# Performance work log

Hardware: AMD Instinct MI355X
Metric: run time of the kernel (lower is better)

The kernel has to match this reference:

```python
import jax, jax.numpy as jnp
import numpy as np

BATCH_SIZE = 4096          # B; representation has 2B rows
TEMPERATURE = 0.5


def setup_inputs() -> dict:
    key = jax.random.key(0)
    k1, k2, k3 = jax.random.split(key, 3)
    representation = jax.random.normal(k1, (2 * BATCH_SIZE, 128), dtype=jnp.float32)
    xrecon = jax.random.normal(k2, (2 * BATCH_SIZE, 512), dtype=jnp.float32)
    xorig = jax.random.normal(k3, (2 * BATCH_SIZE, 512), dtype=jnp.float32)
    return {"representation": representation, "xrecon": xrecon, "xorig": xorig}


def _xneg_loss(representation, batch_size, temperature):
    # Cosine similarity matrix [2B, 2B]
    n = representation / (jnp.linalg.norm(representation, axis=-1, keepdims=True) + 1e-8)
    sim = n @ n.T  # [2B, 2B]
    sim = sim / temperature
    two_b = 2 * batch_size
    # Positives: diag(sim, +B) then diag(sim, -B) -> [2B]
    l_pos = jnp.diagonal(sim, offset=batch_size)
    r_pos = jnp.diagonal(sim, offset=-batch_size)
    positives = jnp.concatenate([l_pos, r_pos])  # [2B]
    # NT-Xent: logits row i = [pos_i] + (row i minus diag and minus pos entry).
    # The union of {pos_i} and negatives_i is row i with only the main diagonal
    # removed, so CE with label 0 equals: -pos_i + logsumexp(row_i \ {diag}).
    neg_inf = jnp.finfo(sim.dtype).min
    eye = jnp.eye(two_b, dtype=bool)
    sim_no_diag = jnp.where(eye, neg_inf, sim)
    lse = jax.nn.logsumexp(sim_no_diag, axis=1)  # [2B]
    loss_sum = jnp.sum(lse - positives)           # CrossEntropyLoss(reduction='sum')
    return loss_sum / two_b


def reference(representation, xrecon, xorig):
    # reconstruction=True -> MSELoss (mean reduction)
    recon_loss = jnp.mean((xrecon - xorig) ** 2)
    loss = recon_loss
    # contrastive_loss=True
    closs = _xneg_loss(representation, BATCH_SIZE, TEMPERATURE)
    loss = loss + closs
    # distance_loss=True: MSE between the two halves of representation
    zi, zj = representation[:BATCH_SIZE], representation[BATCH_SIZE:]
    zrecon_loss = jnp.mean((zi - zj) ** 2)
    loss = loss + zrecon_loss
    return (loss, closs, recon_loss, zrecon_loss)
```

## Files before the change

kernel.cpp:

```cpp
#include <hip/hip_runtime.h>
#include <math.h>

#define BATCH 4096
#define NROWS (2 * BATCH)
#define D 128
#define DX 512

constexpr int NSPLIT = 8;
constexpr int NT = 8;
constexpr int SLOTS = NSPLIT * 2;

#define SCALE 1.698644f

#define WS_PART   0
#define WS_RECONP 131072
#define WS_ZRECP  (WS_RECONP + 512)
#define WS_POSP   (WS_ZRECP + 256)
#define WS_LSEP   (WS_POSP + 256)
#define WS_NBF8   (WS_LSEP + 64)

typedef float f32x16 __attribute__((ext_vector_type(16)));
typedef long long i64;
typedef unsigned char u8;
typedef unsigned short u16;

__device__ __forceinline__ float wave_reduce(float v) {
    #pragma unroll
    for (int o = 32; o > 0; o >>= 1) v += __shfl_xor(v, o);
    return v;
}

__global__ __launch_bounds__(256) void k_prep(const float* __restrict__ rep,
                                              float* __restrict__ ws) {
    const int w = threadIdx.x >> 6, l = threadIdx.x & 63;
    const int wg = blockIdx.x * 4 + w;
    u8* nbf8 = (u8*)(ws + WS_NBF8);
    const int chunk = l >> 2, el = (l & 3) * 2;
    float zacc = 0.f, pacc = 0.f;
    #pragma unroll
    for (int p = 0; p < 4; ++p) {
        const int i = wg + p * 1024;
        float2 a = *reinterpret_cast<const float2*>(rep + i * D + l * 2);
        float2 b = *reinterpret_cast<const float2*>(rep + (i + BATCH) * D + l * 2);
        float dx = a.x - b.x, dy = a.y - b.y;
        float sa  = wave_reduce(a.x * a.x + a.y * a.y);
        float sb  = wave_reduce(b.x * b.x + b.y * b.y);
        float sab = wave_reduce(a.x * b.x + a.y * b.y);
        float sd  = wave_reduce(dx * dx + dy * dy);
        float ia = 1.0f / (sqrtf(sa) + 1e-8f);
        float ib = 1.0f / (sqrtf(sb) + 1e-8f);
        zacc += sd;
        pacc += sab * ia * ib;
        int pka = __builtin_amdgcn_cvt_pk_fp8_f32(a.x * ia * SCALE,
                                                  a.y * ia * SCALE, 0, false);
        int pkb = __builtin_amdgcn_cvt_pk_fp8_f32(b.x * ib * SCALE,
                                                  b.y * ib * SCALE, 0, false);
        *reinterpret_cast<u16*>(
            nbf8 + ((size_t)chunk * NROWS + i) * 8 + el) = (u16)pka;
        *reinterpret_cast<u16*>(
            nbf8 + ((size_t)chunk * NROWS + i + BATCH) * 8 + el) = (u16)pkb;
    }
    __shared__ float shz[4], shp[4];
    if (l == 0) { shz[w] = zacc; shp[w] = pacc; }
    __syncthreads();
    if (threadIdx.x == 0) {
        ws[WS_ZRECP + blockIdx.x] = shz[0] + shz[1] + shz[2] + shz[3];
        ws[WS_POSP + blockIdx.x] = 4.0f * (shp[0] + shp[1] + shp[2] + shp[3]);
    }
}

__global__ __launch_bounds__(256, 2) void k_lse(const float4* __restrict__ xr,
                                                const float4* __restrict__ xo,
                                                float* __restrict__ ws) {
    const u8* __restrict__ nbf8 = (const u8*)(ws + WS_NBF8);
    const int tid = threadIdx.x;
    const int w = tid >> 6, l = tid & 63;
    const int wr = w >> 1, wc = w & 1;
    const int rblk = blockIdx.x;
    const int split = blockIdx.y;
    const int R0 = rblk * 128;
    const int fid = rblk + 64 * split;

    i64 afrag[2][8];
    #pragma unroll
    for (int rb = 0; rb < 2; ++rb) {
        const int lr = R0 + wr * 64 + rb * 32 + (l & 31);
        #pragma unroll
        for (int s = 0; s < 8; ++s) {
            const int c = 2 * s + (l >> 5);
            afrag[rb][s] = *reinterpret_cast<const i64*>(
                nbf8 + ((size_t)c * NROWS + lr) * 8);
        }
    }

    i64 bufA[16], bufB[16];
    float4 raA, rbA, raB, rbB;
    float sumexp[2][16] = {};
    float racc = 0.f;

    auto loadB = [&](i64 (&buf)[16], int t) {
        const int lc = split * (NT * 128) + t * 128 + wc * 64 + (l & 31);
        #pragma unroll
        for (int s = 0; s < 8; ++s) {
            const int c = 2 * s + (l >> 5);
            const u8* base = nbf8 + (size_t)c * NROWS * 8;
            buf[2 * s]     = *reinterpret_cast<const i64*>(base + (size_t)lc * 8);
            buf[2 * s + 1] = *reinterpret_cast<const i64*>(base + (size_t)(lc + 32) * 8);
        }
    };

    auto tile = [&](i64 (&buf)[16], int t, float4 ra, float4 rb2) {
        const int C0 = split * (NT * 128) + t * 128;
        const bool diagt = (C0 == R0);
        f32x16 acc[2][2] = {};
        #pragma unroll
        for (int s = 0; s < 8; ++s) {
            acc[0][0] = __builtin_amdgcn_mfma_f32_32x32x16_fp8_fp8(
                afrag[0][s], buf[2 * s], acc[0][0], 0, 0, 0);
            acc[0][1] = __builtin_amdgcn_mfma_f32_32x32x16_fp8_fp8(
                afrag[0][s], buf[2 * s + 1], acc[0][1], 0, 0, 0);
            acc[1][0] = __builtin_amdgcn_mfma_f32_32x32x16_fp8_fp8(
                afrag[1][s], buf[2 * s], acc[1][0], 0, 0, 0);
            acc[1][1] = __builtin_amdgcn_mfma_f32_32x32x16_fp8_fp8(
                afrag[1][s], buf[2 * s + 1], acc[1][1], 0, 0, 0);
        }
        {
            float dx = ra.x - rb2.x, dy = ra.y - rb2.y;
            float dz = ra.z - rb2.z, dw2 = ra.w - rb2.w;
            racc += dx * dx + dy * dy + dz * dz + dw2 * dw2;
        }
        #pragma unroll
        for (int rb = 0; rb < 2; ++rb) {
            #pragma unroll
            for (int cb = 0; cb < 2; ++cb) {
                const bool dmask = diagt && ((2 * wr + rb) == (2 * wc + cb));
                #pragma unroll
                for (int r = 0; r < 16; ++r) {
                    float e = __builtin_amdgcn_exp2f(acc[rb][cb][r]);
                    if (dmask) {
                        const int rrow = (r & 3) + 8 * (r >> 2) + 4 * (l >> 5);
                        if (rrow == (l & 31)) e = 0.0f;
                    }
                    sumexp[rb][r] += e;
                }
            }
        }
    };

    loadB(bufA, 0);
    {
        const int ri = fid * 2048 + tid;
        raA = xr[ri]; rbA = xo[ri];
    }

    #pragma unroll
    for (int tt = 0; tt < NT; tt += 2) {
        if (tt + 1 < NT) {
            loadB(bufB, tt + 1);
            const int ri = fid * 2048 + (tt + 1) * 256 + tid;
            raB = xr[ri]; rbB = xo[ri];
        }
        tile(bufA, tt, raA, rbA);
        if (tt + 2 < NT) {
            loadB(bufA, tt + 2);
            const int ri = fid * 2048 + (tt + 2) * 256 + tid;
            raA = xr[ri]; rbA = xo[ri];
        }
        if (tt + 1 < NT) tile(bufB, tt + 1, raB, rbB);
    }

    #pragma unroll
    for (int rb = 0; rb < 2; ++rb) {
        #pragma unroll
        for (int r = 0; r < 16; ++r) {
            float v = sumexp[rb][r];
            #pragma unroll
            for (int m = 1; m <= 16; m <<= 1) v += __shfl_xor(v, m);
            sumexp[rb][r] = v;
        }
    }
    if ((l & 31) == 0) {
        #pragma unroll
        for (int rb = 0; rb < 2; ++rb) {
            #pragma unroll
            for (int r = 0; r < 16; ++r) {
                const int row = R0 + wr * 64 + rb * 32
                              + (r & 3) + 8 * (r >> 2) + 4 * (l >> 5);
                ws[WS_PART + row * SLOTS + split * 2 + wc] = sumexp[rb][r];
            }
        }
    }

    racc = wave_reduce(racc);
    __shared__ float shr[4];
    if (l == 0) shr[w] = racc;
    __syncthreads();
    if (tid == 0) ws[WS_RECONP + fid] = shr[0] + shr[1] + shr[2] + shr[3];
}

__global__ __launch_bounds__(256) void k_rowlse(float* __restrict__ ws) {
    const int q = blockIdx.x, tid = threadIdx.x;
    const int j = tid & 127, h = tid >> 7;
    const int row = q * 128 + j;
    float s = 0.f;
    #pragma unroll
    for (int ss = 0; ss < SLOTS / 2; ++ss)
        s += ws[WS_PART + row * SLOTS + 2 * ss + h];
    __shared__ float red[128];
    if (h) red[j] = s;
    __syncthreads();
    float lg = 0.f;
    if (!h) lg = logf(s + red[j]);
    lg = wave_reduce(lg);
    __shared__ float sh[4];
    const int w = tid >> 6, l = tid & 63;
    if (l == 0) sh[w] = lg;
    __syncthreads();
    if (tid == 0) ws[WS_LSEP + q] = sh[0] + sh[1] + sh[2] + sh[3];
}

__global__ __launch_bounds__(256) void k_combine(const float* __restrict__ ws,
                                                 float* __restrict__ out) {
    const int tid = threadIdx.x;
    float lacc = (tid < 64) ? ws[WS_LSEP + tid] : 0.f;
    float racc = ws[WS_RECONP + tid] + ws[WS_RECONP + 256 + tid];
    float zacc = ws[WS_ZRECP + tid];
    float pacc = ws[WS_POSP + tid];

    lacc = wave_reduce(lacc);
    racc = wave_reduce(racc);
    zacc = wave_reduce(zacc);
    pacc = wave_reduce(pacc);

    __shared__ float sh[4][4];
    const int w = tid >> 6, l = tid & 63;
    if (l == 0) { sh[0][w] = lacc; sh[1][w] = racc; sh[2][w] = zacc; sh[3][w] = pacc; }
    __syncthreads();
    if (tid == 0) {
        float lse = sh[0][0] + sh[0][1] + sh[0][2] + sh[0][3];
        float rec = (sh[1][0] + sh[1][1] + sh[1][2] + sh[1][3]) / (float)(NROWS * DX);
        float zre = (sh[2][0] + sh[2][1] + sh[2][2] + sh[2][3]) / (float)(BATCH * D);
        float pos = sh[3][0] + sh[3][1] + sh[3][2] + sh[3][3];
        float closs = (lse - pos) / (float)NROWS;
        out[0] = rec + closs + zre;
        out[1] = closs;
        out[2] = rec;
        out[3] = zre;
    }
}

extern "C" void kernel_launch(void* const* d_in, const int* in_sizes, int n_in,
                              void* d_out, int out_size, void* d_ws, size_t ws_size,
                              hipStream_t stream) {
    const float* rep = (const float*)d_in[0];
    const float4* xr = (const float4*)d_in[1];
    const float4* xo = (const float4*)d_in[2];
    float* out = (float*)d_out;
    float* ws = (float*)d_ws;

    k_prep<<<256, 256, 0, stream>>>(rep, ws);
    dim3 grid(64, NSPLIT);
    k_lse<<<grid, 256, 0, stream>>>(xr, xo, ws);
    k_rowlse<<<64, 256, 0, stream>>>(ws);
    k_combine<<<1, 256, 0, stream>>>(ws, out);
}
```

Before: 33.44 us.

## Software-pipeline MFMA and exp epilogue at half-tile granularity

Splits each 128-column tile into two 64-column halves, each with its own B-fragment buffer and accumulator pair. It interleaves the MFMAs of one half with the exp/sum epilogue of the previous half, so matrix and transcendental units overlap instead of running back to back. The B prefetch buffers shrink from 16 to 8 i64 each, but two live accumulator sets add register pressure under launch_bounds(256,2).

```diff
diff --git a/kernel.cpp b/kernel.cpp
--- a/kernel.cpp
+++ b/kernel.cpp
@@ -86,87 +86,86 @@
     for (int rb = 0; rb < 2; ++rb) {
         const int lr = R0 + wr * 64 + rb * 32 + (l & 31);
         #pragma unroll
-        for (int s = 0; s < 8; ++s) {
-            const int c = 2 * s + (l >> 5);
-            afrag[rb][s] = *reinterpret_cast<const i64*>(
+        for (int k = 0; k < 8; ++k) {
+            const int c = 2 * k + (l >> 5);
+            afrag[rb][k] = *reinterpret_cast<const i64*>(
                 nbf8 + ((size_t)c * NROWS + lr) * 8);
         }
     }
 
-    i64 bufA[16], bufB[16];
-    float4 raA, rbA, raB, rbB;
+    i64 bufA[8], bufB[8];
+    f32x16 accA[2], accB[2];
+    float4 ra, rb2;
     float sumexp[2][16] = {};
     float racc = 0.f;
 
-    auto loadB = [&](i64 (&buf)[16], int t) {
-        const int lc = split * (NT * 128) + t * 128 + wc * 64 + (l & 31);
-        #pragma unroll
-        for (int s = 0; s < 8; ++s) {
-            const int c = 2 * s + (l >> 5);
-            const u8* base = nbf8 + (size_t)c * NROWS * 8;
-            buf[2 * s]     = *reinterpret_cast<const i64*>(base + (size_t)lc * 8);
-            buf[2 * s + 1] = *reinterpret_cast<const i64*>(base + (size_t)(lc + 32) * 8);
+    auto loadB = [&](i64 (&buf)[8], int s) {
+        const int lc = split * (NT * 128) + (s >> 1) * 128 + wc * 64
+                     + (s & 1) * 32 + (l & 31);
+        #pragma unroll
+        for (int k = 0; k < 8; ++k) {
+            const int c = 2 * k + (l >> 5);
+            buf[k] = *reinterpret_cast<const i64*>(
+                nbf8 + ((size_t)c * NROWS + lc) * 8);
         }
     };
 
-    auto tile = [&](i64 (&buf)[16], int t, float4 ra, float4 rb2) {
-        const int C0 = split * (NT * 128) + t * 128;
-        const bool diagt = (C0 == R0);
-        f32x16 acc[2][2] = {};
-        #pragma unroll
-        for (int s = 0; s < 8; ++s) {
-            acc[0][0] = __builtin_amdgcn_mfma_f32_32x32x16_fp8_fp8(
-                afrag[0][s], buf[2 * s], acc[0][0], 0, 0, 0);
-            acc[0][1] = __builtin_amdgcn_mfma_f32_32x32x16_fp8_fp8(
-                afrag[0][s], buf[2 * s + 1], acc[0][1], 0, 0, 0);
-            acc[1][0] = __builtin_amdgcn_mfma_f32_32x32x16_fp8_fp8(
-                afrag[1][s], buf[2 * s], acc[1][0], 0, 0, 0);
-            acc[1][1] = __builtin_amdgcn_mfma_f32_32x32x16_fp8_fp8(
-                afrag[1][s], buf[2 * s + 1], acc[1][1], 0, 0, 0);
-        }
+    auto mfmaH = [&](i64 (&buf)[8], f32x16 (&acc)[2]) {
+        acc[0] = (f32x16)(0.f);
+        acc[1] = (f32x16)(0.f);
+        #pragma unroll
+        for (int k = 0; k < 8; ++k) {
+            acc[0] = __builtin_amdgcn_mfma_f32_32x32x16_fp8_fp8(
+                afrag[0][k], buf[k], acc[0], 0, 0, 0);
+            acc[1] = __builtin_amdgcn_mfma_f32_32x32x16_fp8_fp8(
+                afrag[1][k], buf[k], acc[1], 0, 0, 0);
+        }
+    };
+
+    auto expH = [&](f32x16 (&acc)[2], int s) {
+        const int t = s >> 1, cb = s & 1;
+        const bool diagt = (split * NT + t) == rblk;
+        #pragma unroll
+        for (int rb = 0; rb < 2; ++rb) {
+            const bool dmask = diagt && ((2 * wr + rb) == (2 * wc + cb));
+            #pragma unroll
+            for (int r = 0; r < 16; ++r) {
+                float e = __builtin_amdgcn_exp2f(acc[rb][r]);
+                if (dmask) {
+                    const int rrow = (r & 3) + 8 * (r >> 2) + 4 * (l >> 5);
+                    if (rrow == (l & 31)) e = 0.0f;
+                }
+                sumexp[rb][r] += e;
+            }
+        }
+    };
+
+    loadB(bufA, 0);
+    loadB(bufB, 1);
+    {
+        const int ri = fid * 2048 + tid;
+        ra = xr[ri]; rb2 = xo[ri];
+    }
+    mfmaH(bufA, accA);
+
+    #pragma unroll
+    for (int s = 0; s < 16; s += 2) {
+        const int k = s >> 1;
+        if (s + 2 < 16) loadB(bufA, s + 2);
+        mfmaH(bufB, accB);
         {
             float dx = ra.x - rb2.x, dy = ra.y - rb2.y;
             float dz = ra.z - rb2.z, dw2 = ra.w - rb2.w;
             racc += dx * dx + dy * dy + dz * dz + dw2 * dw2;
         }
-        #pragma unroll
-        for (int rb = 0; rb < 2; ++rb) {
-            #pragma unroll
-            for (int cb = 0; cb < 2; ++cb) {
-                const bool dmask = diagt && ((2 * wr + rb) == (2 * wc + cb));
-                #pragma unroll
-                for (int r = 0; r < 16; ++r) {
-                    float e = __builtin_amdgcn_exp2f(acc[rb][cb][r]);
-                    if (dmask) {
-                        const int rrow = (r & 3) + 8 * (r >> 2) + 4 * (l >> 5);
-                        if (rrow == (l & 31)) e = 0.0f;
-                    }
-                    sumexp[rb][r] += e;
-                }
-            }
-        }
-    };
-
-    loadB(bufA, 0);
-    {
-        const int ri = fid * 2048 + tid;
-        raA = xr[ri]; rbA = xo[ri];
-    }
-
-    #pragma unroll
-    for (int tt = 0; tt < NT; tt += 2) {
-        if (tt + 1 < NT) {
-            loadB(bufB, tt + 1);
-            const int ri = fid * 2048 + (tt + 1) * 256 + tid;
-            raB = xr[ri]; rbB = xo[ri];
-        }
-        tile(bufA, tt, raA, rbA);
-        if (tt + 2 < NT) {
-            loadB(bufA, tt + 2);
-            const int ri = fid * 2048 + (tt + 2) * 256 + tid;
-            raA = xr[ri]; rbA = xo[ri];
-        }
-        if (tt + 1 < NT) tile(bufB, tt + 1, raB, rbB);
+        if (k + 1 < 8) {
+            const int ri = fid * 2048 + (k + 1) * 256 + tid;
+            ra = xr[ri]; rb2 = xo[ri];
+        }
+        expH(accA, s);
+        if (s + 3 < 16) loadB(bufB, s + 3);
+        if (s + 2 < 16) mfmaH(bufA, accA);
+        expH(accB, s + 1);
     }
 
     #pragma unroll
```

New measurement: 33.96 us. Within noise of the previous version (+1.6%).

## Repack FP8 normalized rows for 16-byte loads and stagger tile order

Applied to the files above, without the earlier changes.

The FP8 normalized-representation buffer is re-laid out so that each lane fetches two consecutive K-chunks with one 16-byte vector load instead of two 8-byte loads. The split and row-block indices are folded into a 1D grid so neighbouring blocks share row tiles. Each wave starts its column-tile loop at a different offset to spread memory traffic. This aims to cut load instruction count and improve cache locality, at the cost of a more intricate indexing scheme.

```diff
diff --git a/kernel.cpp b/kernel.cpp
--- a/kernel.cpp
+++ b/kernel.cpp
@@ -18,9 +18,12 @@
 #define WS_POSP   (WS_ZRECP + 256)
 #define WS_LSEP   (WS_POSP + 256)
 #define WS_NBF8   (WS_LSEP + 64)
+#define HREG 524288
+#define JSTR 131072
 
 typedef float f32x16 __attribute__((ext_vector_type(16)));
 typedef long long i64;
+typedef i64 i64x2 __attribute__((ext_vector_type(2)));
 typedef unsigned char u8;
 typedef unsigned short u16;
 
@@ -35,7 +38,9 @@
     const int w = threadIdx.x >> 6, l = threadIdx.x & 63;
     const int wg = blockIdx.x * 4 + w;
     u8* nbf8 = (u8*)(ws + WS_NBF8);
-    const int chunk = l >> 2, el = (l & 3) * 2;
+    const int c = l >> 2;
+    const int boff = (c & 1) * HREG + (c >> 2) * JSTR + ((c >> 1) & 1) * 8
+                   + (l & 3) * 2;
     float zacc = 0.f, pacc = 0.f;
     #pragma unroll
     for (int p = 0; p < 4; ++p) {
@@ -55,10 +60,8 @@
                                                   a.y * ia * SCALE, 0, false);
         int pkb = __builtin_amdgcn_cvt_pk_fp8_f32(b.x * ib * SCALE,
                                                   b.y * ib * SCALE, 0, false);
-        *reinterpret_cast<u16*>(
-            nbf8 + ((size_t)chunk * NROWS + i) * 8 + el) = (u16)pka;
-        *reinterpret_cast<u16*>(
-            nbf8 + ((size_t)chunk * NROWS + i + BATCH) * 8 + el) = (u16)pkb;
+        *reinterpret_cast<u16*>(nbf8 + boff + i * 16) = (u16)pka;
+        *reinterpret_cast<u16*>(nbf8 + boff + (i + BATCH) * 16) = (u16)pkb;
     }
     __shared__ float shz[4], shp[4];
     if (l == 0) { shz[w] = zacc; shp[w] = pacc; }
@@ -76,53 +79,50 @@
     const int tid = threadIdx.x;
     const int w = tid >> 6, l = tid & 63;
     const int wr = w >> 1, wc = w & 1;
-    const int rblk = blockIdx.x;
-    const int split = blockIdx.y;
+    const int rblk = blockIdx.x >> 3;
+    const int split = blockIdx.x & 7;
     const int R0 = rblk * 128;
     const int fid = rblk + 64 * split;
-
-    i64 afrag[2][8];
+    const u8* __restrict__ hbase = nbf8 + (l >> 5) * HREG;
+    const int t0 = (2 * w) & 7;
+
+    i64x2 afr[2][4];
     #pragma unroll
     for (int rb = 0; rb < 2; ++rb) {
         const int lr = R0 + wr * 64 + rb * 32 + (l & 31);
         #pragma unroll
-        for (int s = 0; s < 8; ++s) {
-            const int c = 2 * s + (l >> 5);
-            afrag[rb][s] = *reinterpret_cast<const i64*>(
-                nbf8 + ((size_t)c * NROWS + lr) * 8);
-        }
-    }
-
-    i64 bufA[16], bufB[16];
+        for (int j = 0; j < 4; ++j)
+            afr[rb][j] = *reinterpret_cast<const i64x2*>(hbase + j * JSTR + lr * 16);
+    }
+
+    i64x2 bufA[8], bufB[8];
     float4 raA, rbA, raB, rbB;
     float sumexp[2][16] = {};
     float racc = 0.f;
 
-    auto loadB = [&](i64 (&buf)[16], int t) {
+    auto loadB = [&](i64x2 (&buf)[8], int t) {
         const int lc = split * (NT * 128) + t * 128 + wc * 64 + (l & 31);
         #pragma unroll
-        for (int s = 0; s < 8; ++s) {
-            const int c = 2 * s + (l >> 5);
-            const u8* base = nbf8 + (size_t)c * NROWS * 8;
-            buf[2 * s]     = *reinterpret_cast<const i64*>(base + (size_t)lc * 8);
-            buf[2 * s + 1] = *reinterpret_cast<const i64*>(base + (size_t)(lc + 32) * 8);
+        for (int j = 0; j < 4; ++j) {
+            buf[j]     = *reinterpret_cast<const i64x2*>(hbase + j * JSTR + lc * 16);
+            buf[4 + j] = *reinterpret_cast<const i64x2*>(
+                hbase + j * JSTR + (lc + 32) * 16);
         }
     };
 
-    auto tile = [&](i64 (&buf)[16], int t, float4 ra, float4 rb2) {
-        const int C0 = split * (NT * 128) + t * 128;
-        const bool diagt = (C0 == R0);
+    auto tile = [&](i64x2 (&buf)[8], int t, float4 ra, float4 rb2) {
+        const bool diagt = (split * NT + t) == rblk;
         f32x16 acc[2][2] = {};
         #pragma unroll
-        for (int s = 0; s < 8; ++s) {
-            acc[0][0] = __builtin_amdgcn_mfma_f32_32x32x16_fp8_fp8(
-                afrag[0][s], buf[2 * s], acc[0][0], 0, 0, 0);
-            acc[0][1] = __builtin_amdgcn_mfma_f32_32x32x16_fp8_fp8(
-                afrag[0][s], buf[2 * s + 1], acc[0][1], 0, 0, 0);
-            acc[1][0] = __builtin_amdgcn_mfma_f32_32x32x16_fp8_fp8(
-                afrag[1][s], buf[2 * s], acc[1][0], 0, 0, 0);
-            acc[1][1] = __builtin_amdgcn_mfma_f32_32x32x16_fp8_fp8(
-                afrag[1][s], buf[2 * s + 1], acc[1][1], 0, 0, 0);
+        for (int k = 0; k < 8; ++k) {
+            const i64 a0 = afr[0][k >> 1][k & 1];
+            const i64 a1 = afr[1][k >> 1][k & 1];
+            const i64 b0 = buf[k >> 1][k & 1];
+            const i64 b1 = buf[4 + (k >> 1)][k & 1];
+            acc[0][0] = __builtin_amdgcn_mfma_f32_32x32x16_fp8_fp8(a0, b0, acc[0][0], 0, 0, 0);
+            acc[0][1] = __builtin_amdgcn_mfma_f32_32x32x16_fp8_fp8(a0, b1, acc[0][1], 0, 0, 0);
+            acc[1][0] = __builtin_amdgcn_mfma_f32_32x32x16_fp8_fp8(a1, b0, acc[1][0], 0, 0, 0);
+            acc[1][1] = __builtin_amdgcn_mfma_f32_32x32x16_fp8_fp8(a1, b1, acc[1][1], 0, 0, 0);
         }
         {
             float dx = ra.x - rb2.x, dy = ra.y - rb2.y;
@@ -147,26 +147,28 @@
         }
     };
 
-    loadB(bufA, 0);
+    loadB(bufA, t0);
     {
-        const int ri = fid * 2048 + tid;
+        const int ri = fid * 2048 + t0 * 256 + tid;
         raA = xr[ri]; rbA = xo[ri];
     }
 
     #pragma unroll
     for (int tt = 0; tt < NT; tt += 2) {
+        const int tB = (tt + 1 + t0) & 7;
+        const int tA2 = (tt + 2 + t0) & 7;
         if (tt + 1 < NT) {
-            loadB(bufB, tt + 1);
-            const int ri = fid * 2048 + (tt + 1) * 256 + tid;
+            loadB(bufB, tB);
+            const int ri = fid * 2048 + tB * 256 + tid;
             raB = xr[ri]; rbB = xo[ri];
         }
-        tile(bufA, tt, raA, rbA);
+        tile(bufA, (tt + t0) & 7, raA, rbA);
         if (tt + 2 < NT) {
-            loadB(bufA, tt + 2);
-            const int ri = fid * 2048 + (tt + 2) * 256 + tid;
+            loadB(bufA, tA2);
+            const int ri = fid * 2048 + tA2 * 256 + tid;
             raA = xr[ri]; rbA = xo[ri];
         }
-        if (tt + 1 < NT) tile(bufB, tt + 1, raB, rbB);
+        if (tt + 1 < NT) tile(bufB, tB, raB, rbB);
     }
 
     #pragma unroll
@@ -259,8 +261,7 @@
     float* ws = (float*)d_ws;
 
     k_prep<<<256, 256, 0, stream>>>(rep, ws);
-    dim3 grid(64, NSPLIT);
-    k_lse<<<grid, 256, 0, stream>>>(xr, xo, ws);
+    k_lse<<<512, 256, 0, stream>>>(xr, xo, ws);
     k_rowlse<<<64, 256, 0, stream>>>(ws);
     k_combine<<<1, 256, 0, stream>>>(ws, out);
 }
```

Measured after the change: 39.66 us. 18.6% more time.
